# Kernel tuning notes

Hardware: AMD Instinct MI355X
Metric: run time of the kernel (lower is better)

## Reference

```python
import jax, jax.numpy as jnp
import numpy as np

NUM_HEADS = 8
HEAD_SIZE = 64
INPUT = 512
OUT = NUM_HEADS * HEAD_SIZE
B, S = 4, 2048


def setup_inputs() -> dict:
    key = jax.random.key(0)
    ks = jax.random.split(key, 6)
    return {
        "key": jax.random.normal(ks[0], (B, S, INPUT), dtype=jnp.float32),
        "key_mask": jnp.zeros((B, 1, 1, S), dtype=jnp.float32),
        "query": jax.random.normal(ks[1], (B, S, INPUT), dtype=jnp.float32),
        "value": jax.random.normal(ks[2], (B, S, INPUT), dtype=jnp.float32),
        "wq": jax.random.normal(ks[3], (INPUT, OUT), dtype=jnp.float32) * (INPUT ** -0.5),
        "wk": jax.random.normal(ks[4], (INPUT, OUT), dtype=jnp.float32) * (INPUT ** -0.5),
        "wv": jax.random.normal(ks[5], (INPUT, OUT), dtype=jnp.float32) * (INPUT ** -0.5),
    }


def _split_heads(x):
    # [B, S, H*hd] -> [B, H, S, hd]
    b, s, _ = x.shape
    return x.reshape(b, s, NUM_HEADS, HEAD_SIZE).transpose(0, 2, 1, 3)


def reference(key, key_mask, query, value, wq, wk, wv):
    q = _split_heads(query @ wq)   # [B,H,S,hd]
    k = _split_heads(key @ wk)
    v = _split_heads(value @ wv)
    scale = 1.0 / jnp.sqrt(jnp.asarray(HEAD_SIZE, q.dtype))
    logits = jnp.einsum('bhqd,bhkd->bhqk', q, k) * scale + key_mask
    attn = jax.nn.softmax(logits, axis=-1)
    out = jnp.einsum('bhqk,bhkd->bhqd', attn, v)  # [B,H,S,hd]
    out = out.transpose(0, 2, 1, 3).reshape(out.shape[0], out.shape[2], OUT)
    return out
```

## Files before the change

### kernel.cpp

```cpp
#include <hip/hip_runtime.h>

typedef _Float16 f16;
typedef f16 f16x8 __attribute__((ext_vector_type(8)));
typedef f16 f16x4 __attribute__((ext_vector_type(4)));
typedef f16 f16x2 __attribute__((ext_vector_type(2)));
typedef float f32x4 __attribute__((ext_vector_type(4)));
typedef unsigned int u32;

#define MFMA16(a, b, c) __builtin_amdgcn_mfma_f32_16x16x32_f16(a, b, c, 0, 0, 0)

#define BATCH 4
#define NHEADS 8
#define HDIM 64
#define SEQ 2048
#define DIN 512
#define DOUT 512
#define LOG2E 1.44269504f
#define C1 0.18033688f

__device__ __forceinline__ void gl_lds16(const void* g, const void* l) {
  __builtin_amdgcn_global_load_lds(
      (const __attribute__((address_space(1))) u32*)g,
      (__attribute__((address_space(3))) u32*)l, 16, 0, 0);
}

__device__ __forceinline__ float fexp2(float x) {
  float r;
  asm("v_exp_f32 %0, %1" : "=v"(r) : "v"(x));
  return r;
}

__device__ __forceinline__ f16x2 pk2(float a, float b) {
  return __builtin_bit_cast(f16x2, __builtin_amdgcn_cvt_pkrtz(a, b));
}

__device__ __forceinline__ f16x4 pk4(float a, float b, float c, float d) {
  f16x2 u0 = pk2(a, b), u1 = pk2(c, d);
  f16x4 r;
  r[0] = u0[0]; r[1] = u0[1]; r[2] = u1[0]; r[3] = u1[1];
  return r;
}

__global__ __launch_bounds__(256) void prep_w(
    const float* __restrict__ wq, const float* __restrict__ wk,
    const float* __restrict__ wv, f16* __restrict__ wT) {
  __shared__ float tile[64][65];
  const float* w = blockIdx.z == 0 ? wq : (blockIdx.z == 1 ? wk : wv);
  f16* out = wT + (size_t)blockIdx.z * DIN * DOUT;
  int k0 = blockIdx.x * 64, n0 = blockIdx.y * 64;
  int t = threadIdx.x;
  int c = t & 63, rb = t >> 6;
#pragma unroll
  for (int ph = 0; ph < 16; ++ph) {
    int r = ph * 4 + rb;
    tile[r][c] = w[(size_t)(k0 + r) * DOUT + n0 + c];
  }
  __syncthreads();
#pragma unroll
  for (int ph = 0; ph < 16; ++ph) {
    int n = ph * 4 + rb;
    out[(size_t)(n0 + n) * DIN + k0 + c] = (f16)tile[c][n];
  }
}

__global__ __launch_bounds__(256, 3) void qkv_gemm(
    const float* __restrict__ xq, const float* __restrict__ xk,
    const float* __restrict__ xv, const f16* __restrict__ wT,
    f16* __restrict__ Qo, f16* __restrict__ Ko, f16* __restrict__ Vt) {
  __shared__ __attribute__((aligned(16))) f16 smem[16384];
  f16* As = smem;
  f16* Bs = smem + 8192;
  f16* CT = smem;

  int gemm = blockIdx.z;
  const float* x = gemm == 0 ? xq : (gemm == 1 ? xk : xv);
  const f16* wt = wT + (size_t)gemm * DIN * DOUT;
  int bx = blockIdx.x;
  int m0 = (bx & 63) * 128, n0 = (bx >> 6) * 128;
  int t = threadIdx.x, w = t >> 6, lane = t & 63;
  int lr = lane & 15, lq = lane >> 4;
  int wm = (w >> 1) * 64, wn = (w & 1) * 64;

  int tr = t >> 4, tc = t & 15;
  const float* xg = x + (size_t)(m0 + tr) * DIN + tc * 4;
  int aw[8];
#pragma unroll
  for (int ph = 0; ph < 8; ++ph) {
    int r = tr + 16 * ph;
    int phys = (tc >> 1) ^ (r & 7);
    aw[ph] = r * 64 + phys * 8 + (tc & 1) * 4;
  }

  int srow = lane >> 3;
  int schunk = (lane & 7) ^ srow;
  const f16* gb[4];
  const f16* lbb[4];
#pragma unroll
  for (int j = 0; j < 4; ++j) {
    int br = w * 32 + j * 8;
    gb[j] = wt + (size_t)(n0 + br + srow) * DIN + schunk * 8;
    lbb[j] = &Bs[__builtin_amdgcn_readfirstlane(br * 64)];
  }
  int xo0 = ((0 * 4 + lq) ^ (lr & 7)) * 8;
  int xo1 = ((1 * 4 + lq) ^ (lr & 7)) * 8;

  f32x4 zero = {0.f, 0.f, 0.f, 0.f};
  f32x4 acc[4][4];
#pragma unroll
  for (int i = 0; i < 4; ++i)
#pragma unroll
    for (int j = 0; j < 4; ++j) acc[i][j] = zero;

  for (int k0 = 0; k0 < DIN; k0 += 64) {
    __syncthreads();
#pragma unroll
    for (int j = 0; j < 4; ++j) gl_lds16(gb[j] + k0, lbb[j]);
#pragma unroll
    for (int ph = 0; ph < 8; ++ph) {
      float4 a = *(const float4*)(xg + (size_t)ph * 16 * DIN + k0);
      *(f16x4*)&As[aw[ph]] = pk4(a.x, a.y, a.z, a.w);
    }
    __syncthreads();
#pragma unroll
    for (int c = 0; c < 2; ++c) {
      int xo = c ? xo1 : xo0;
      f16x8 xf[4], wf[4];
#pragma unroll
      for (int i = 0; i < 4; ++i)
        xf[i] = *(const f16x8*)&As[(wm + i * 16 + lr) * 64 + xo];
#pragma unroll
      for (int i = 0; i < 4; ++i)
        wf[i] = *(const f16x8*)&Bs[(wn + i * 16 + lr) * 64 + xo];
      if (gemm == 2) {
#pragma unroll
        for (int i = 0; i < 4; ++i)
#pragma unroll
          for (int j = 0; j < 4; ++j)
            acc[i][j] = MFMA16(xf[i], wf[j], acc[i][j]);
      } else {
#pragma unroll
        for (int i = 0; i < 4; ++i)
#pragma unroll
          for (int j = 0; j < 4; ++j)
            acc[i][j] = MFMA16(wf[i], xf[j], acc[i][j]);
      }
    }
  }

  __syncthreads();
  int b_ = m0 >> 11;
  int sl = m0 & 2047;

  if (gemm == 2) {
#pragma unroll
    for (int i = 0; i < 4; ++i) {
#pragma unroll
      for (int j = 0; j < 4; ++j) {
        int d = wn + j * 16 + lr;
        int lc = (wm >> 3) + i * 2 + (lq >> 1);
        int phys = lc ^ lr;
        *(f16x4*)&CT[d * 128 + phys * 8 + (lq & 1) * 4] =
            pk4(acc[i][j][0], acc[i][j][1], acc[i][j][2], acc[i][j][3]);
      }
    }
    __syncthreads();
    int tid16 = t & 15;
#pragma unroll
    for (int ph = 0; ph < 8; ++ph) {
      int d = ph * 16 + (t >> 4);
      int phys = tid16 ^ (d & 15);
      f16x8 vv = *(const f16x8*)&CT[d * 128 + phys * 8];
      int hgl = (n0 + d) >> 6, dd = (n0 + d) & 63;
      *(f16x8*)&Vt[(((size_t)b_ * NHEADS + hgl) * HDIM + dd) * SEQ + sl +
                   tid16 * 8] = vv;
    }
  } else {
    f16* O = gemm == 0 ? Qo : Ko;
    float sc = gemm == 0 ? C1 : 1.0f;
#pragma unroll
    for (int i = 0; i < 4; ++i) {
#pragma unroll
      for (int j = 0; j < 4; ++j) {
        int s = wm + j * 16 + lr;
        int lc = (wn >> 3) + i * 2 + (lq >> 1);
        int phys = lc ^ lr;
        *(f16x4*)&CT[s * 128 + phys * 8 + (lq & 1) * 4] =
            pk4(acc[i][j][0] * sc, acc[i][j][1] * sc, acc[i][j][2] * sc,
                acc[i][j][3] * sc);
      }
    }
    __syncthreads();
    int tid8 = t & 7;
    int hh = (t >> 3) & 1;
#pragma unroll
    for (int ph = 0; ph < 8; ++ph) {
      int s = ph * 16 + (t >> 4);
      int lc = hh * 8 + tid8;
      int phys = lc ^ (s & 15);
      f16x8 vv = *(const f16x8*)&CT[s * 128 + phys * 8];
      int hgl = (n0 >> 6) + hh;
      *(f16x8*)&O[(((size_t)b_ * NHEADS + hgl) * SEQ + sl + s) * HDIM +
                  tid8 * 8] = vv;
    }
  }
}

__global__ __launch_bounds__(256, 2) void flash_attn(
    const f16* __restrict__ Q, const f16* __restrict__ K,
    const f16* __restrict__ Vt, const float* __restrict__ mask,
    float* __restrict__ out) {
  __shared__ __attribute__((aligned(16))) f16 Ks[128 * 64];
  __shared__ __attribute__((aligned(16))) f16 Vs[64 * 128];
  __shared__ __attribute__((aligned(16))) f16 Ps[128 * 136];

  int bh = blockIdx.x, q0 = blockIdx.y * 128;
  int b = bh >> 3, h = bh & 7;
  int t = threadIdx.x, w = t >> 6, lane = t & 63;
  int lr = lane & 15, lq = lane >> 4;

  const f16* Qg = Q + (size_t)bh * SEQ * HDIM;
  const f16* Kg = K + (size_t)bh * SEQ * HDIM;
  const f16* Vg = Vt + (size_t)bh * HDIM * SEQ;
  const float* mg = mask + (size_t)b * SEQ;

  f16x8 qf[2][2];
#pragma unroll
  for (int u = 0; u < 2; ++u)
#pragma unroll
    for (int c = 0; c < 2; ++c)
      qf[u][c] = *(const f16x8*)(Qg +
                                 (size_t)(q0 + w * 32 + u * 16 + lr) * HDIM +
                                 c * 32 + lq * 8);

  int krow = lane >> 3;
  int kchunk = (lane & 7) ^ krow;
  const f16* gk[4];
  const f16* gv[4];
  const f16* lk[4];
  const f16* lv[4];
#pragma unroll
  for (int j = 0; j < 4; ++j) {
    int kbr = w * 32 + j * 8;
    gk[j] = Kg + (size_t)(kbr + krow) * HDIM + kchunk * 8;
    lk[j] = &Ks[__builtin_amdgcn_readfirstlane(kbr * 64)];
    int vbr = w * 16 + j * 4;
    int vchunk = (lane & 15) ^ (j * 4 + lq);
    gv[j] = Vg + (size_t)(vbr + lq) * SEQ + vchunk * 8;
    lv[j] = &Vs[__builtin_amdgcn_readfirstlane(vbr * 128)];
  }
  int xk0 = ((0 * 4 + lq) ^ (lr & 7)) * 8;
  int xk1 = ((1 * 4 + lq) ^ (lr & 7)) * 8;

  f32x4 zero = {0.f, 0.f, 0.f, 0.f};
  f32x4 acc[2][4];
#pragma unroll
  for (int u = 0; u < 2; ++u)
#pragma unroll
    for (int i = 0; i < 4; ++i) acc[u][i] = zero;
  float lsum[2] = {0.f, 0.f};

  for (int k0 = 0; k0 < SEQ; k0 += 128) {
    __syncthreads();
#pragma unroll
    for (int j = 0; j < 4; ++j) {
      gl_lds16(gk[j] + (size_t)k0 * HDIM, lk[j]);
      gl_lds16(gv[j] + k0, lv[j]);
    }
    __syncthreads();

    f32x4 s[2][8];
#pragma unroll
    for (int nt = 0; nt < 8; ++nt) {
      f16x8 kf0 = *(const f16x8*)&Ks[(nt * 16 + lr) * 64 + xk0];
      f16x8 kf1 = *(const f16x8*)&Ks[(nt * 16 + lr) * 64 + xk1];
      s[0][nt] = MFMA16(kf0, qf[0][0], zero);
      s[0][nt] = MFMA16(kf1, qf[0][1], s[0][nt]);
      s[1][nt] = MFMA16(kf0, qf[1][0], zero);
      s[1][nt] = MFMA16(kf1, qf[1][1], s[1][nt]);
    }

#pragma unroll
    for (int nt = 0; nt < 8; ++nt) {
      float4 mk = *(const float4*)(mg + k0 + nt * 16 + lq * 4);
#pragma unroll
      for (int u = 0; u < 2; ++u) {
        float p0 = fexp2(fmaf(mk.x, LOG2E, s[u][nt][0]));
        float p1 = fexp2(fmaf(mk.y, LOG2E, s[u][nt][1]));
        float p2 = fexp2(fmaf(mk.z, LOG2E, s[u][nt][2]));
        float p3 = fexp2(fmaf(mk.w, LOG2E, s[u][nt][3]));
        lsum[u] += (p0 + p1) + (p2 + p3);
        *(f16x4*)&Ps[(w * 32 + u * 16 + lr) * 136 + nt * 16 + lq * 4] =
            pk4(p0, p1, p2, p3);
      }
    }

#pragma unroll
    for (int ks = 0; ks < 4; ++ks) {
      f16x8 ap0 = *(const f16x8*)&Ps[(w * 32 + lr) * 136 + ks * 32 + lq * 8];
      f16x8 ap1 =
          *(const f16x8*)&Ps[(w * 32 + 16 + lr) * 136 + ks * 32 + lq * 8];
#pragma unroll
      for (int dt = 0; dt < 4; ++dt) {
        f16x8 bv = *(const f16x8*)&Vs[(dt * 16 + lr) * 128 +
                                      (((ks * 4 + lq) ^ lr) * 8)];
        acc[0][dt] = MFMA16(ap0, bv, acc[0][dt]);
        acc[1][dt] = MFMA16(ap1, bv, acc[1][dt]);
      }
    }
  }

#pragma unroll
  for (int u = 0; u < 2; ++u) {
    float l = lsum[u];
    l += __shfl_xor(l, 16);
    l += __shfl_xor(l, 32);
    float inv = 1.f / l;
    float iv[4];
#pragma unroll
    for (int r = 0; r < 4; ++r) iv[r] = __shfl(inv, lq * 4 + r);
#pragma unroll
    for (int dt = 0; dt < 4; ++dt) {
#pragma unroll
      for (int r = 0; r < 4; ++r) {
        int q = q0 + w * 32 + u * 16 + lq * 4 + r;
        int d = h * HDIM + dt * 16 + lr;
        out[((size_t)b * SEQ + q) * DOUT + d] = acc[u][dt][r] * iv[r];
      }
    }
  }
}

extern "C" void kernel_launch(void* const* d_in, const int* in_sizes, int n_in,
                              void* d_out, int out_size, void* d_ws,
                              size_t ws_size, hipStream_t stream) {
  const float* key = (const float*)d_in[0];
  const float* key_mask = (const float*)d_in[1];
  const float* query = (const float*)d_in[2];
  const float* value = (const float*)d_in[3];
  const float* wq = (const float*)d_in[4];
  const float* wk = (const float*)d_in[5];
  const float* wv = (const float*)d_in[6];
  float* out = (float*)d_out;

  char* ws = (char*)d_ws;
  f16* Qws = (f16*)(ws);
  f16* Kws = (f16*)(ws + 8388608);
  f16* Vtws = (f16*)(ws + 16777216);
  f16* wT = (f16*)(ws + 25165824);

  prep_w<<<dim3(8, 8, 3), 256, 0, stream>>>(wq, wk, wv, wT);
  qkv_gemm<<<dim3(256, 1, 3), 256, 0, stream>>>(query, key, value, wT, Qws,
                                                Kws, Vtws);
  flash_attn<<<dim3(32, 16), 256, 0, stream>>>(Qws, Kws, Vtws, key_mask, out);
}
```

Baseline: 187.2 us.

## Overlap K/V tile loads with compute and stage mask in LDS

Restructures the flash-attention loop so the next K tile is loaded into LDS while the softmax runs, and the next V tile is loaded after the PV MFMAs, with explicit vmcnt waits and barriers in place of two full syncthreads per iteration. The whole mask row is preloaded into LDS once, replacing per-iteration global mask reads. s_setprio is raised around the MFMA phases. This adds 8KB of LDS, which can lower occupancy, and relies on careful vmcnt accounting, so it risks races if the counts are wrong.

```diff
diff --git a/kernel.cpp b/kernel.cpp
--- a/kernel.cpp
+++ b/kernel.cpp
@@ -212,6 +212,7 @@
   __shared__ __attribute__((aligned(16))) f16 Ks[128 * 64];
   __shared__ __attribute__((aligned(16))) f16 Vs[64 * 128];
   __shared__ __attribute__((aligned(16))) f16 Ps[128 * 136];
+  __shared__ __attribute__((aligned(16))) float Ms[SEQ];
 
   int bh = blockIdx.x, q0 = blockIdx.y * 128;
   int b = bh >> 3, h = bh & 7;
@@ -259,16 +260,27 @@
     for (int i = 0; i < 4; ++i) acc[u][i] = zero;
   float lsum[2] = {0.f, 0.f};
 
-  for (int k0 = 0; k0 < SEQ; k0 += 128) {
-    __syncthreads();
-#pragma unroll
-    for (int j = 0; j < 4; ++j) {
-      gl_lds16(gk[j] + (size_t)k0 * HDIM, lk[j]);
-      gl_lds16(gv[j] + k0, lv[j]);
-    }
-    __syncthreads();
+  {
+    int c0 = w * 512;
+    gl_lds16(mg + c0 + lane * 4, &Ms[__builtin_amdgcn_readfirstlane(c0)]);
+    gl_lds16(mg + c0 + 256 + lane * 4,
+             &Ms[__builtin_amdgcn_readfirstlane(c0 + 256)]);
+  }
+#pragma unroll
+  for (int j = 0; j < 4; ++j) {
+    gl_lds16(gk[j], lk[j]);
+    gl_lds16(gv[j], lv[j]);
+  }
+  asm volatile("s_waitcnt vmcnt(0)" ::: "memory");
+  __builtin_amdgcn_sched_barrier(0);
+  __builtin_amdgcn_s_barrier();
+  __builtin_amdgcn_sched_barrier(0);
+
+  for (int it = 0; it < 16; ++it) {
+    int k0 = it * 128;
 
     f32x4 s[2][8];
+    __builtin_amdgcn_s_setprio(1);
 #pragma unroll
     for (int nt = 0; nt < 8; ++nt) {
       f16x8 kf0 = *(const f16x8*)&Ks[(nt * 16 + lr) * 64 + xk0];
@@ -278,10 +290,21 @@
       s[1][nt] = MFMA16(kf0, qf[1][0], zero);
       s[1][nt] = MFMA16(kf1, qf[1][1], s[1][nt]);
     }
+    __builtin_amdgcn_s_setprio(0);
+
+    asm volatile("s_waitcnt vmcnt(0)" ::: "memory");
+    __builtin_amdgcn_sched_barrier(0);
+    __builtin_amdgcn_s_barrier();
+    __builtin_amdgcn_sched_barrier(0);
+    if (it < 15) {
+#pragma unroll
+      for (int j = 0; j < 4; ++j)
+        gl_lds16(gk[j] + (size_t)(k0 + 128) * HDIM, lk[j]);
+    }
 
 #pragma unroll
     for (int nt = 0; nt < 8; ++nt) {
-      float4 mk = *(const float4*)(mg + k0 + nt * 16 + lq * 4);
+      float4 mk = *(const float4*)&Ms[k0 + nt * 16 + lq * 4];
 #pragma unroll
       for (int u = 0; u < 2; ++u) {
         float p0 = fexp2(fmaf(mk.x, LOG2E, s[u][nt][0]));
@@ -294,6 +317,7 @@
       }
     }
 
+    __builtin_amdgcn_s_setprio(1);
 #pragma unroll
     for (int ks = 0; ks < 4; ++ks) {
       f16x8 ap0 = *(const f16x8*)&Ps[(w * 32 + lr) * 136 + ks * 32 + lq * 8];
@@ -306,6 +330,19 @@
         acc[0][dt] = MFMA16(ap0, bv, acc[0][dt]);
         acc[1][dt] = MFMA16(ap1, bv, acc[1][dt]);
       }
+    }
+    __builtin_amdgcn_s_setprio(0);
+
+    if (it < 15) {
+      __builtin_amdgcn_sched_barrier(0);
+      __builtin_amdgcn_s_barrier();
+      __builtin_amdgcn_sched_barrier(0);
+#pragma unroll
+      for (int j = 0; j < 4; ++j) gl_lds16(gv[j] + k0 + 128, lv[j]);
+      asm volatile("s_waitcnt vmcnt(4)" ::: "memory");
+      __builtin_amdgcn_sched_barrier(0);
+      __builtin_amdgcn_s_barrier();
+      __builtin_amdgcn_sched_barrier(0);
     }
   }
 
```

New measurement: 181.9 us. 1.03x faster.
